# Optimization experiments

Measured on AMD Instinct MI355X. Metric: run time of the kernel, lower is better.

## Reference

```python
import jax, jax.numpy as jnp
import numpy as np


def setup_inputs() -> dict:
    key = jax.random.key(0)
    k1, k2 = jax.random.split(key)
    p_hat = jax.random.normal(k1, (16384, 3), dtype=jnp.float32)
    p = jax.random.normal(k2, (16384, 3), dtype=jnp.float32)
    return {"p_hat": p_hat, "p": p}


def reference(p_hat, p):
    # squared pairwise L2 distances: ||a-b||^2 = ||a||^2 + ||b||^2 - 2 a.b
    a2 = jnp.sum(p_hat * p_hat, axis=-1)            # [N]
    b2 = jnp.sum(p * p, axis=-1)                    # [M]
    cross = p_hat @ p.T                             # [N, M]
    d2 = jnp.maximum(a2[:, None] + b2[None, :] - 2.0 * cross, 0.0)
    # Chamfer: mean of col-mins (min over dim 0) + mean of row-mins (min over dim 1)
    return jnp.mean(jnp.min(d2, axis=0)) + jnp.mean(jnp.min(d2, axis=1))
```

## Files before the change

### kernel.cpp

```cpp
#include <hip/hip_runtime.h>

#define N 16384
#define TPB 256
#define INF_BITS 0x7F800000

#define NT32 (N / 32)
#define MT 4
#define NSTRIP (NT32 / MT)
#define NJSPLIT 8
#define JW (NT32 / NJSPLIT)
#define NWAVES (2 * NSTRIP * NJSPLIT)
#define NBLK_MFMA (NWAVES / 4)
#define FRAG_U4 (NT32 * 64)
#define WS_NEED_MFMA (4ull * FRAG_U4 * sizeof(uint4) + 2ull * N * sizeof(int))

using bf16x8 = __attribute__((ext_vector_type(8))) short;
using fx16   = __attribute__((ext_vector_type(16))) float;

__device__ __forceinline__ unsigned short bf16_rn(float f) {
    unsigned u = __float_as_uint(f);
    u += 0x7FFFu + ((u >> 16) & 1u);
    return (unsigned short)(u >> 16);
}
__device__ __forceinline__ float bf16f(unsigned short h) {
    return __uint_as_float(((unsigned)h) << 16);
}
__device__ __forceinline__ uint4 pack8(const unsigned short* a) {
    return make_uint4((unsigned)a[0] | ((unsigned)a[1] << 16),
                      (unsigned)a[2] | ((unsigned)a[3] << 16),
                      (unsigned)a[4] | ((unsigned)a[5] << 16),
                      (unsigned)a[6] | ((unsigned)a[7] << 16));
}

__global__ void pack_mfma(const float* __restrict__ p_hat, const float* __restrict__ p,
                          uint4* __restrict__ frags, int* __restrict__ minbuf)
{
    int idx = blockIdx.x * blockDim.x + threadIdx.x;
    if (idx >= 2 * N) return;
    minbuf[idx] = INF_BITS;
    const float* src = (idx < N) ? p_hat : p;
    int i = (idx < N) ? idx : idx - N;
    float x = src[3*i+0], y = src[3*i+1], z = src[3*i+2];

    unsigned short xh = bf16_rn(x), yh = bf16_rn(y), zh = bf16_rn(z);
    unsigned short xl = bf16_rn(x - bf16f(xh));
    unsigned short yl = bf16_rn(y - bf16f(yh));
    unsigned short zl = bf16_rn(z - bf16f(zh));
    float s = __builtin_fmaf(x, x, __builtin_fmaf(y, y, z * z));
    unsigned short sh = bf16_rn(s), sl = bf16_rn(s - bf16f(sh));
    unsigned short m2xh = bf16_rn(-2.0f * bf16f(xh)), m2xl = bf16_rn(-2.0f * bf16f(xl));
    unsigned short m2yh = bf16_rn(-2.0f * bf16f(yh)), m2yl = bf16_rn(-2.0f * bf16f(yl));
    unsigned short m2zh = bf16_rn(-2.0f * bf16f(zh)), m2zl = bf16_rn(-2.0f * bf16f(zl));
    const unsigned short one = 0x3F80;

    unsigned short q[16] = { m2xh, m2xh, m2xl, m2xl, m2yh, m2yh, m2yl, m2yl,
                             m2zh, m2zh, m2zl, m2zl, sh, sl, one, one };
    unsigned short r[16] = { xh, xl, xh, xl, yh, yl, yh, yl,
                             zh, zl, zh, zl, one, one, sh, sl };

    uint4* Qa = frags + ((idx < N) ? 0 : FRAG_U4);
    uint4* Ra = frags + 2 * FRAG_U4 + ((idx < N) ? 0 : FRAG_U4);
    int t = i >> 5, rr = i & 31;
    Qa[t * 64 +      rr] = pack8(q);
    Qa[t * 64 + 32 + rr] = pack8(q + 8);
    Ra[t * 64 +      rr] = pack8(r);
    Ra[t * 64 + 32 + rr] = pack8(r + 8);
}

__global__ void __launch_bounds__(TPB, 2) chamfer_mfma(const uint4* __restrict__ frags,
                                                       int* __restrict__ minbuf)
{
    int lane = threadIdx.x & 63;
    int wid  = blockIdx.x * 4 + (int)(threadIdx.x >> 6);
    int strip  = wid & (NSTRIP - 1);
    int jsplit = (wid >> 7) & (NJSPLIT - 1);
    int pass   = wid >> 10;

    const uint4* Q = frags + (pass ? FRAG_U4 : 0);
    const uint4* R = frags + 2 * FRAG_U4 + (pass ? 0 : FRAG_U4);

    bf16x8 A[MT];
#pragma unroll
    for (int m = 0; m < MT; ++m)
        A[m] = __builtin_bit_cast(bf16x8, Q[(strip * MT + m) * 64 + lane]);

    fx16 zf;
#pragma unroll
    for (int r2 = 0; r2 < 16; ++r2) zf[r2] = 0.0f;
    fx16 rmin[MT];
#pragma unroll
    for (int m = 0; m < MT; ++m)
#pragma unroll
        for (int r2 = 0; r2 < 16; ++r2) rmin[m][r2] = __builtin_inff();

    const uint4* Rj = R + jsplit * (JW * 64) + lane;
    uint4 ca = Rj[0];
    uint4 cb = Rj[64];
    for (int jj = 0; jj < JW; jj += 2) {
        int n2 = (jj + 2 < JW) ? (jj + 2) : 0;
        int n3 = (jj + 2 < JW) ? (jj + 3) : 1;
        uint4 na = Rj[n2 * 64];
        uint4 nb = Rj[n3 * 64];
        bf16x8 Ba = __builtin_bit_cast(bf16x8, ca);
        bf16x8 Bb = __builtin_bit_cast(bf16x8, cb);
#pragma unroll
        for (int m = 0; m < MT; ++m) {
            fx16 da = __builtin_amdgcn_mfma_f32_32x32x16_bf16(A[m], Ba, zf, 0, 0, 0);
            fx16 db = __builtin_amdgcn_mfma_f32_32x32x16_bf16(A[m], Bb, zf, 0, 0, 0);
#pragma unroll
            for (int r2 = 0; r2 < 16; ++r2) {
                rmin[m][r2] = fminf(rmin[m][r2], fminf(da[r2], db[r2]));
            }
        }
        ca = na; cb = nb;
    }

    int rowbase = pass * N + strip * (MT * 32) + 4 * (lane >> 5);
#pragma unroll
    for (int m = 0; m < MT; ++m) {
#pragma unroll
        for (int r2 = 0; r2 < 16; ++r2) {
            float v = rmin[m][r2];
            v = fminf(v, __shfl_xor(v, 1));
            v = fminf(v, __shfl_xor(v, 2));
            v = fminf(v, __shfl_xor(v, 4));
            v = fminf(v, __shfl_xor(v, 8));
            v = fminf(v, __shfl_xor(v, 16));
            if ((lane & 31) == 0) {
                int row = rowbase + m * 32 + (r2 & 3) + 8 * (r2 >> 2);
                atomicMin(&minbuf[row], __float_as_int(fmaxf(v, 0.0f)));
            }
        }
    }
}

__global__ void __launch_bounds__(1024) reduce_kernel(const int* __restrict__ minbuf,
                                                      float* __restrict__ out) {
    const int4* mb4 = (const int4*)minbuf;
    float s = 0.0f;
#pragma unroll
    for (int k = 0; k < (2 * N / 4) / 1024; ++k) {
        int4 v = mb4[k * 1024 + threadIdx.x];
        s += __int_as_float(v.x) + __int_as_float(v.y) +
             __int_as_float(v.z) + __int_as_float(v.w);
    }
    for (int off = 32; off > 0; off >>= 1) s += __shfl_down(s, off, 64);
    __shared__ float partial[1024 / 64];
    int lane = threadIdx.x & 63;
    int wid  = threadIdx.x >> 6;
    if (lane == 0) partial[wid] = s;
    __syncthreads();
    if (threadIdx.x == 0) {
        float t = 0.0f;
        for (int w = 0; w < 1024 / 64; ++w) t += partial[w];
        out[0] = t / (float)N;
    }
}

#define OQPT 4
#define OQTILE (TPB * OQPT)
#define ONQT (N / OQTILE)
#define OSPLIT 64
#define OCHUNK (N / OSPLIT)
#define OGRID (2 * OSPLIT * ONQT)

__global__ void pack_old(const float* __restrict__ p_hat, const float* __restrict__ p,
                         float4* __restrict__ q4, int* __restrict__ minbuf) {
    int idx = blockIdx.x * blockDim.x + threadIdx.x;
    if (idx >= 2 * N) return;
    const float* src = (idx < N) ? p_hat : p;
    int k = (idx < N) ? idx : idx - N;
    float x = src[3*k+0], y = src[3*k+1], z = src[3*k+2];
    q4[idx] = make_float4(x, y, z, x*x + y*y + z*z);
    minbuf[idx] = INF_BITS;
}

__global__ void __launch_bounds__(TPB) chamfer_old(const float4* __restrict__ q4,
                                                   int* __restrict__ minbuf) {
    int b = blockIdx.x;
    int dir = b & 1;
    int rest = b >> 1;
    int jc = rest & (OSPLIT - 1);
    int qt = rest >> 6;
    const float4* __restrict__ qp = q4 + (dir ? N : 0);
    const float4* __restrict__ rp = q4 + (dir ? 0 : N);
    int ibase = qt * OQTILE + (int)threadIdx.x;
    float m2x[OQPT], m2y[OQPT], m2z[OQPT], qw[OQPT], vmin[OQPT];
#pragma unroll
    for (int q = 0; q < OQPT; ++q) {
        float4 qq = qp[ibase + q * TPB];
        m2x[q] = -2.0f * qq.x; m2y[q] = -2.0f * qq.y; m2z[q] = -2.0f * qq.z;
        qw[q] = qq.w; vmin[q] = __builtin_inff();
    }
    int j0 = jc * OCHUNK;
    float4 ra = rp[j0];
    float4 rb = rp[j0 + 1];
#pragma unroll 2
    for (int j = j0; j < j0 + OCHUNK; j += 2) {
        float4 na = rp[j + 2];
        float4 nb = rp[j + 3];
        float raw = ra.w, rbw = rb.w;
#pragma unroll
        for (int q = 0; q < OQPT; ++q) {
            float ta = __builtin_fmaf(ra.x, m2x[q],
                       __builtin_fmaf(ra.y, m2y[q],
                       __builtin_fmaf(ra.z, m2z[q], raw)));
            float tb = __builtin_fmaf(rb.x, m2x[q],
                       __builtin_fmaf(rb.y, m2y[q],
                       __builtin_fmaf(rb.z, m2z[q], rbw)));
            vmin[q] = fminf(vmin[q], fminf(ta, tb));
        }
        ra = na; rb = nb;
    }
#pragma unroll
    for (int q = 0; q < OQPT; ++q) {
        float m = fmaxf(vmin[q] + qw[q], 0.0f);
        atomicMin(&minbuf[dir * N + ibase + q * TPB], __float_as_int(m));
    }
}

extern "C" void kernel_launch(void* const* d_in, const int* in_sizes, int n_in,
                              void* d_out, int out_size, void* d_ws, size_t ws_size,
                              hipStream_t stream) {
    const float* p_hat = (const float*)d_in[0];
    const float* p     = (const float*)d_in[1];
    float* out = (float*)d_out;
    if (ws_size >= WS_NEED_MFMA) {
        uint4* frags = (uint4*)d_ws;
        int* minbuf  = (int*)((char*)d_ws + 4ull * FRAG_U4 * sizeof(uint4));
        pack_mfma<<<(2 * N + TPB - 1) / TPB, TPB, 0, stream>>>(p_hat, p, frags, minbuf);
        chamfer_mfma<<<NBLK_MFMA, TPB, 0, stream>>>(frags, minbuf);
        reduce_kernel<<<1, 1024, 0, stream>>>(minbuf, out);
    } else {
        float4* q4  = (float4*)d_ws;
        int* minbuf = (int*)((char*)d_ws + 2 * N * sizeof(float4));
        pack_old<<<(2 * N + TPB - 1) / TPB, TPB, 0, stream>>>(p_hat, p, q4, minbuf);
        chamfer_old<<<OGRID, TPB, 0, stream>>>(q4, minbuf);
        reduce_kernel<<<1, 1024, 0, stream>>>(minbuf, out);
    }
}
```

Measured before the change: 89.83 us.

## Stage shared B tiles in LDS via async global_load_lds double buffering

The four waves in a block share the same column split, so B fragments are now cooperatively loaded into a double-buffered LDS tile using direct global-to-LDS loads. Each wave reads them from LDS instead of fetching them from global memory. This cuts redundant global/L2 traffic four-fold but adds a block barrier per chunk of 8 tiles and LDS read traffic.

```diff
diff --git a/kernel.cpp b/kernel.cpp
--- a/kernel.cpp
+++ b/kernel.cpp
@@ -11,6 +11,8 @@
 #define JW (NT32 / NJSPLIT)
 #define NWAVES (2 * NSTRIP * NJSPLIT)
 #define NBLK_MFMA (NWAVES / 4)
+#define CHTILES 8
+#define NCHUNK (JW / CHTILES)
 #define FRAG_U4 (NT32 * 64)
 #define WS_NEED_MFMA (4ull * FRAG_U4 * sizeof(uint4) + 2ull * N * sizeof(int))
 
@@ -70,8 +72,11 @@
 __global__ void __launch_bounds__(TPB, 2) chamfer_mfma(const uint4* __restrict__ frags,
                                                        int* __restrict__ minbuf)
 {
+    __shared__ uint4 sB[2][CHTILES * 64];
+
     int lane = threadIdx.x & 63;
-    int wid  = blockIdx.x * 4 + (int)(threadIdx.x >> 6);
+    int w    = (int)(threadIdx.x >> 6);
+    int wid  = blockIdx.x * 4 + w;
     int strip  = wid & (NSTRIP - 1);
     int jsplit = (wid >> 7) & (NJSPLIT - 1);
     int pass   = wid >> 10;
@@ -93,26 +98,46 @@
 #pragma unroll
         for (int r2 = 0; r2 < 16; ++r2) rmin[m][r2] = __builtin_inff();
 
-    const uint4* Rj = R + jsplit * (JW * 64) + lane;
-    uint4 ca = Rj[0];
-    uint4 cb = Rj[64];
-    for (int jj = 0; jj < JW; jj += 2) {
-        int n2 = (jj + 2 < JW) ? (jj + 2) : 0;
-        int n3 = (jj + 2 < JW) ? (jj + 3) : 1;
-        uint4 na = Rj[n2 * 64];
-        uint4 nb = Rj[n3 * 64];
-        bf16x8 Ba = __builtin_bit_cast(bf16x8, ca);
-        bf16x8 Bb = __builtin_bit_cast(bf16x8, cb);
-#pragma unroll
-        for (int m = 0; m < MT; ++m) {
-            fx16 da = __builtin_amdgcn_mfma_f32_32x32x16_bf16(A[m], Ba, zf, 0, 0, 0);
-            fx16 db = __builtin_amdgcn_mfma_f32_32x32x16_bf16(A[m], Bb, zf, 0, 0, 0);
-#pragma unroll
-            for (int r2 = 0; r2 < 16; ++r2) {
-                rmin[m][r2] = fminf(rmin[m][r2], fminf(da[r2], db[r2]));
+    const uint4* Rj = R + jsplit * (JW * 64);
+
+    {
+        const uint4* g = Rj + (w * 2) * 64 + lane;
+        __builtin_amdgcn_global_load_lds(
+            (const __attribute__((address_space(1))) void*)g,
+            (__attribute__((address_space(3))) void*)&sB[0][(w * 2) * 64], 16, 0, 0);
+        __builtin_amdgcn_global_load_lds(
+            (const __attribute__((address_space(1))) void*)(g + 64),
+            (__attribute__((address_space(3))) void*)&sB[0][(w * 2 + 1) * 64], 16, 0, 0);
+    }
+    __syncthreads();
+
+    for (int c = 0; c < NCHUNK; ++c) {
+        int cur = c & 1, nb = cur ^ 1;
+        int nc = (c + 1) & (NCHUNK - 1);
+        const uint4* g = Rj + (nc * CHTILES + w * 2) * 64 + lane;
+        __builtin_amdgcn_global_load_lds(
+            (const __attribute__((address_space(1))) void*)g,
+            (__attribute__((address_space(3))) void*)&sB[nb][(w * 2) * 64], 16, 0, 0);
+        __builtin_amdgcn_global_load_lds(
+            (const __attribute__((address_space(1))) void*)(g + 64),
+            (__attribute__((address_space(3))) void*)&sB[nb][(w * 2 + 1) * 64], 16, 0, 0);
+
+#pragma unroll
+        for (int t = 0; t < CHTILES; t += 2) {
+            uint4 ca = sB[cur][t * 64 + lane];
+            uint4 cb = sB[cur][(t + 1) * 64 + lane];
+            bf16x8 Ba = __builtin_bit_cast(bf16x8, ca);
+            bf16x8 Bb = __builtin_bit_cast(bf16x8, cb);
+#pragma unroll
+            for (int m = 0; m < MT; ++m) {
+                fx16 da = __builtin_amdgcn_mfma_f32_32x32x16_bf16(A[m], Ba, zf, 0, 0, 0);
+                fx16 db = __builtin_amdgcn_mfma_f32_32x32x16_bf16(A[m], Bb, zf, 0, 0, 0);
+#pragma unroll
+                for (int r2 = 0; r2 < 16; ++r2)
+                    rmin[m][r2] = fminf(rmin[m][r2], fminf(da[r2], db[r2]));
             }
         }
-        ca = na; cb = nb;
+        __syncthreads();
     }
 
     int rowbase = pass * N + strip * (MT * 32) + 4 * (lane >> 5);
```

After: 105.8 us. 1.18x slower.

## Fuse final reduction into MFMA kernel via last-block counter; stage pack loads in LDS

Applied to the files above, without the earlier changes.

Drops the separate reduce kernel launch: each chamfer block increments a global done counter after its atomics, and the last block to finish sums the min buffer and writes the output. The pack kernel now loads the xyz coordinates through shared memory with coalesced float4 reads instead of strided scalar loads, and it resets the counter. This removes one launch and its gap, at the cost of a fence and atomic per block and a serial reduction done by a single 256-thread block.

```diff
diff --git a/kernel.cpp b/kernel.cpp
--- a/kernel.cpp
+++ b/kernel.cpp
@@ -12,7 +12,7 @@
 #define NWAVES (2 * NSTRIP * NJSPLIT)
 #define NBLK_MFMA (NWAVES / 4)
 #define FRAG_U4 (NT32 * 64)
-#define WS_NEED_MFMA (4ull * FRAG_U4 * sizeof(uint4) + 2ull * N * sizeof(int))
+#define WS_NEED_MFMA (4ull * FRAG_U4 * sizeof(uint4) + 2ull * N * sizeof(int) + 16)
 
 using bf16x8 = __attribute__((ext_vector_type(8))) short;
 using fx16   = __attribute__((ext_vector_type(16))) float;
@@ -33,14 +33,24 @@
 }
 
 __global__ void pack_mfma(const float* __restrict__ p_hat, const float* __restrict__ p,
-                          uint4* __restrict__ frags, int* __restrict__ minbuf)
+                          uint4* __restrict__ frags, int* __restrict__ minbuf,
+                          int* __restrict__ done)
 {
-    int idx = blockIdx.x * blockDim.x + threadIdx.x;
-    if (idx >= 2 * N) return;
+    __shared__ float sIn[TPB * 3];
+    int t   = (int)threadIdx.x;
+    int idx = (int)blockIdx.x * TPB + t;
+    if (idx == 0) *done = 0;
     minbuf[idx] = INF_BITS;
+
     const float* src = (idx < N) ? p_hat : p;
+    int fbase = ((int)blockIdx.x & 63) * (TPB * 3);
+    if (t < (TPB * 3) / 4) {
+        float4 v = *(const float4*)(src + fbase + t * 4);
+        *(float4*)&sIn[t * 4] = v;
+    }
+    __syncthreads();
+    float x = sIn[3 * t + 0], y = sIn[3 * t + 1], z = sIn[3 * t + 2];
     int i = (idx < N) ? idx : idx - N;
-    float x = src[3*i+0], y = src[3*i+1], z = src[3*i+2];
 
     unsigned short xh = bf16_rn(x), yh = bf16_rn(y), zh = bf16_rn(z);
     unsigned short xl = bf16_rn(x - bf16f(xh));
@@ -60,18 +70,21 @@
 
     uint4* Qa = frags + ((idx < N) ? 0 : FRAG_U4);
     uint4* Ra = frags + 2 * FRAG_U4 + ((idx < N) ? 0 : FRAG_U4);
-    int t = i >> 5, rr = i & 31;
-    Qa[t * 64 +      rr] = pack8(q);
-    Qa[t * 64 + 32 + rr] = pack8(q + 8);
-    Ra[t * 64 +      rr] = pack8(r);
-    Ra[t * 64 + 32 + rr] = pack8(r + 8);
+    int tt = i >> 5, rr = i & 31;
+    Qa[tt * 64 +      rr] = pack8(q);
+    Qa[tt * 64 + 32 + rr] = pack8(q + 8);
+    Ra[tt * 64 +      rr] = pack8(r);
+    Ra[tt * 64 + 32 + rr] = pack8(r + 8);
 }
 
 __global__ void __launch_bounds__(TPB, 2) chamfer_mfma(const uint4* __restrict__ frags,
-                                                       int* __restrict__ minbuf)
+                                                       int* __restrict__ minbuf,
+                                                       int* __restrict__ done,
+                                                       float* __restrict__ out)
 {
     int lane = threadIdx.x & 63;
-    int wid  = blockIdx.x * 4 + (int)(threadIdx.x >> 6);
+    int w    = (int)(threadIdx.x >> 6);
+    int wid  = blockIdx.x * 4 + w;
     int strip  = wid & (NSTRIP - 1);
     int jsplit = (wid >> 7) & (NJSPLIT - 1);
     int pass   = wid >> 10;
@@ -132,28 +145,31 @@
             }
         }
     }
-}
-
-__global__ void __launch_bounds__(1024) reduce_kernel(const int* __restrict__ minbuf,
-                                                      float* __restrict__ out) {
-    const int4* mb4 = (const int4*)minbuf;
-    float s = 0.0f;
-#pragma unroll
-    for (int k = 0; k < (2 * N / 4) / 1024; ++k) {
-        int4 v = mb4[k * 1024 + threadIdx.x];
-        s += __int_as_float(v.x) + __int_as_float(v.y) +
-             __int_as_float(v.z) + __int_as_float(v.w);
-    }
-    for (int off = 32; off > 0; off >>= 1) s += __shfl_down(s, off, 64);
-    __shared__ float partial[1024 / 64];
-    int lane = threadIdx.x & 63;
-    int wid  = threadIdx.x >> 6;
-    if (lane == 0) partial[wid] = s;
+
+    __threadfence();
+    __shared__ int isLast;
+    if (threadIdx.x == 0) {
+        int old = atomicAdd(done, 1);
+        isLast = (old == NBLK_MFMA - 1);
+    }
     __syncthreads();
-    if (threadIdx.x == 0) {
-        float t = 0.0f;
-        for (int w = 0; w < 1024 / 64; ++w) t += partial[w];
-        out[0] = t / (float)N;
+    if (isLast) {
+        __threadfence();
+        float s = 0.0f;
+        for (int k = (int)threadIdx.x; k < 2 * N; k += TPB) {
+            int bits = __hip_atomic_load(&minbuf[k], __ATOMIC_RELAXED,
+                                         __HIP_MEMORY_SCOPE_AGENT);
+            s += __int_as_float(bits);
+        }
+        for (int off = 32; off > 0; off >>= 1) s += __shfl_down(s, off, 64);
+        __shared__ float partial[TPB / 64];
+        if ((threadIdx.x & 63) == 0) partial[threadIdx.x >> 6] = s;
+        __syncthreads();
+        if (threadIdx.x == 0) {
+            float tsum = 0.0f;
+            for (int q = 0; q < TPB / 64; ++q) tsum += partial[q];
+            out[0] = tsum / (float)N;
+        }
     }
 }
 
@@ -219,6 +235,29 @@
     }
 }
 
+__global__ void __launch_bounds__(1024) reduce_kernel(const int* __restrict__ minbuf,
+                                                      float* __restrict__ out) {
+    const int4* mb4 = (const int4*)minbuf;
+    float s = 0.0f;
+#pragma unroll
+    for (int k = 0; k < (2 * N / 4) / 1024; ++k) {
+        int4 v = mb4[k * 1024 + threadIdx.x];
+        s += __int_as_float(v.x) + __int_as_float(v.y) +
+             __int_as_float(v.z) + __int_as_float(v.w);
+    }
+    for (int off = 32; off > 0; off >>= 1) s += __shfl_down(s, off, 64);
+    __shared__ float partial[1024 / 64];
+    int lane = threadIdx.x & 63;
+    int wid  = threadIdx.x >> 6;
+    if (lane == 0) partial[wid] = s;
+    __syncthreads();
+    if (threadIdx.x == 0) {
+        float t = 0.0f;
+        for (int w = 0; w < 1024 / 64; ++w) t += partial[w];
+        out[0] = t / (float)N;
+    }
+}
+
 extern "C" void kernel_launch(void* const* d_in, const int* in_sizes, int n_in,
                               void* d_out, int out_size, void* d_ws, size_t ws_size,
                               hipStream_t stream) {
@@ -228,9 +267,9 @@
     if (ws_size >= WS_NEED_MFMA) {
         uint4* frags = (uint4*)d_ws;
         int* minbuf  = (int*)((char*)d_ws + 4ull * FRAG_U4 * sizeof(uint4));
-        pack_mfma<<<(2 * N + TPB - 1) / TPB, TPB, 0, stream>>>(p_hat, p, frags, minbuf);
-        chamfer_mfma<<<NBLK_MFMA, TPB, 0, stream>>>(frags, minbuf);
-        reduce_kernel<<<1, 1024, 0, stream>>>(minbuf, out);
+        int* done    = minbuf + 2 * N;
+        pack_mfma<<<(2 * N) / TPB, TPB, 0, stream>>>(p_hat, p, frags, minbuf, done);
+        chamfer_mfma<<<NBLK_MFMA, TPB, 0, stream>>>(frags, minbuf, done, out);
     } else {
         float4* q4  = (float4*)d_ws;
         int* minbuf = (int*)((char*)d_ws + 2 * N * sizeof(float4));
```

New measurement: 144.9 us. 1.61x slower.
